# Performance work log

Hardware: AMD Instinct MI355X
Metric: run time of the kernel (lower is better)

## Reference

```python
import jax, jax.numpy as jnp
import numpy as np

F = 26            # number of categorical fields
V_FIELD = 8000    # vocab per field
V = F * V_FIELD   # 208000, size of every shared-index table
D_EMB = 16
DNN_IN = F * F * D_EMB  # 10816
H1, H2 = 256, 128
BS = 4096
NUM_DENSE = 13
EPS = 1e-5


def setup_inputs() -> dict:
    key = jax.random.key(0)
    ks = jax.random.split(key, 16)
    def n(k, shape, s=0.05):
        return jax.random.normal(k, shape, dtype=jnp.float32) * s
    return {
        "X_sparse": jax.random.randint(ks[0], (BS, F), 0, V_FIELD, dtype=jnp.int32),
        "X_dense": jax.random.normal(ks[1], (BS, NUM_DENSE), dtype=jnp.float32),
        "fm1_emb": n(ks[2], (V, 1)),
        "bias": jnp.zeros((1,), jnp.float32),
        "fm1_dense_W": n(ks[3], (1, NUM_DENSE)),
        "fm1_dense_b": jnp.zeros((1,), jnp.float32),
        "emb_tables": n(ks[4], (F, V, D_EMB)),  # one table per field (FFM)
        "dense_W": n(ks[5], (DNN_IN, NUM_DENSE)),
        "dense_b": jnp.zeros((DNN_IN,), jnp.float32),
        "W1": n(ks[6], (H1, DNN_IN)),
        "b1": jnp.zeros((H1,), jnp.float32),
        "g1": jnp.ones((H1,), jnp.float32),
        "beta1": jnp.zeros((H1,), jnp.float32),
        "W2": n(ks[7], (H2, H1)),
        "b2": jnp.zeros((H2,), jnp.float32),
        "g2": jnp.ones((H2,), jnp.float32),
        "beta2": jnp.zeros((H2,), jnp.float32),
        "Wout": n(ks[8], (1, H2)),
        "bout": jnp.zeros((1,), jnp.float32),
    }


def _bn(x, g, b):
    # BatchNorm1d in training mode: biased batch statistics
    m = jnp.mean(x, axis=0)
    v = jnp.var(x, axis=0)
    return (x - m) * jax.lax.rsqrt(v + EPS) * g + b


def reference(X_sparse, X_dense, fm1_emb, bias, fm1_dense_W, fm1_dense_b,
              emb_tables, dense_W, dense_b,
              W1, b1, g1, beta1, W2, b2, g2, beta2, Wout, bout):
    offsets = (jnp.arange(F, dtype=X_sparse.dtype) * V_FIELD)[None, :]
    X = X_sparse + offsets                      # [bs, F] global indices

    # FM first order
    fm1 = jnp.sum(fm1_emb[X], axis=1) + bias    # [bs, 1]
    fm1 = fm1 + X_dense @ fm1_dense_W.T + fm1_dense_b

    # FFM second order: E[t, b, f, d] = table t looked up at field f's index
    E = emb_tables[:, X, :]                     # [F, bs, F, d]
    A = jnp.transpose(E, (1, 0, 2, 3))          # [bs, F_table, F_field, d]
    # pair (i<j): xs[j][:, i] * xs[i][:, j] = A[b, i, j] * A[b, j, i]
    P = A * jnp.swapaxes(A, 1, 2)               # [bs, F, F, d]
    mask = jnp.triu(jnp.ones((F, F), jnp.float32), 1)
    fm2 = jnp.einsum('bijd,ij->b', P, mask)[:, None]  # [bs, 1]

    # DNN: concat per-table lookups then flatten -> [bs, F*F*d]
    dnn = A.reshape(A.shape[0], DNN_IN)
    dnn = dnn + jax.nn.relu(X_dense @ dense_W.T + dense_b)
    h = jax.nn.relu(_bn(dnn @ W1.T + b1, g1, beta1))  # dropout is identity (eval)
    h = jax.nn.relu(_bn(h @ W2.T + b2, g2, beta2))
    out = h @ Wout.T + bout
    return jax.nn.sigmoid(fm1 + fm2 + out)
```

## Files before the change

### kernel.cpp

```cpp
#include <hip/hip_runtime.h>

typedef __bf16 bf16x8 __attribute__((ext_vector_type(8)));
typedef float f32x4 __attribute__((ext_vector_type(4)));

#define F_FIELDS 26
#define V_FIELD  8000
#define V_TOT    208000
#define D_EMBD   16
#define DNN_IN   10816
#define BS       4096
#define ND       13
#define H1_DIM   256
#define H2_DIM   128
#define NP1      8

__device__ __forceinline__ unsigned short f2bf(float f) {
  unsigned u = __float_as_uint(f);
  u += 0x7fffu + ((u >> 16) & 1u);
  return (unsigned short)(u >> 16);
}
__device__ __forceinline__ float bf2f(unsigned short h) {
  return __uint_as_float(((unsigned)h) << 16);
}
__device__ __forceinline__ float bflo(unsigned u) { return __uint_as_float(u << 16); }
__device__ __forceinline__ float bfhi(unsigned u) { return __uint_as_float(u & 0xffff0000u); }
__device__ __forceinline__ unsigned packbf(float a, float b) {
  return (unsigned)f2bf(a) | ((unsigned)f2bf(b) << 16);
}

__device__ __forceinline__ void gload16(const void* g, void* l) {
  __builtin_amdgcn_global_load_lds(
      (const __attribute__((address_space(1))) unsigned int*)g,
      (__attribute__((address_space(3))) unsigned int*)l, 16, 0, 0);
}

__device__ __forceinline__ float dot8bf(uint4 a, uint4 b) {
  const unsigned* pa = (const unsigned*)&a;
  const unsigned* pb = (const unsigned*)&b;
  float s = 0.f;
#pragma unroll
  for (int k = 0; k < 4; ++k)
    s += bflo(pa[k]) * bflo(pb[k]) + bfhi(pa[k]) * bfhi(pb[k]);
  return s;
}

__global__ __launch_bounds__(256) void k_gather(
    const int* __restrict__ Xs, const float* __restrict__ emb,
    const float* __restrict__ fm1_emb, const float* __restrict__ bias,
    const float* __restrict__ fm1dW, const float* __restrict__ fm1db,
    const float* __restrict__ Xd,
    const float* __restrict__ W1, const float* __restrict__ W2,
    const float* __restrict__ dW, const float* __restrict__ db_,
    unsigned short* __restrict__ W1b, unsigned short* __restrict__ W2b,
    unsigned short* __restrict__ dWb,
    unsigned short* __restrict__ Abf, float* __restrict__ fm12) {
  const int b = blockIdx.x;
  const int tid = threadIdx.x;
  const int lane = tid & 63, wave = tid >> 6;
  __shared__ int   sidx[F_FIELDS];
  __shared__ float sc1[F_FIELDS];
  __shared__ __align__(16) unsigned short As[676 * 16];
  __shared__ float wred[4];

  if (tid < F_FIELDS) {
    int v = Xs[b * F_FIELDS + tid] + tid * V_FIELD;
    sidx[tid] = v;
    sc1[tid] = fm1_emb[v];
  }
  __syncthreads();

  const int q = tid & 3, rbase = tid >> 2;
  float4 vv[11];
#pragma unroll
  for (int it = 0; it < 11; ++it) {
    int r = rbase + it * 64;
    if (r < 676) {
      int i = r / 26, j = r - i * 26;
      const float* src = emb + ((size_t)i * V_TOT + sidx[j]) * D_EMBD + q * 4;
      vv[it] = *(const float4*)src;
    }
  }
  const int n1 = H1_DIM * DNN_IN, n2 = H2_DIM * H1_DIM;
  for (int t = b * 256 + tid; t < n1 + n2; t += BS * 256) {
    if (t < n1) W1b[t] = f2bf(W1[t]);
    else        W2b[t - n1] = f2bf(W2[t - n1]);
  }
  for (int e = b * 256 + tid; e < DNN_IN; e += BS * 256) {
    unsigned short row[32];
#pragma unroll
    for (int k = 0; k < 13; ++k) row[k] = f2bf(dW[e * 13 + k]);
    row[13] = f2bf(db_[e]);
#pragma unroll
    for (int k = 14; k < 32; ++k) row[k] = 0;
#pragma unroll
    for (int k = 0; k < 32; ++k) dWb[e * 32 + k] = row[k];
  }
#pragma unroll
  for (int it = 0; it < 11; ++it) {
    int r = rbase + it * 64;
    if (r < 676) {
      unsigned lo = packbf(vv[it].x, vv[it].y);
      unsigned hi = packbf(vv[it].z, vv[it].w);
      unsigned long long pk = (unsigned long long)lo |
                              ((unsigned long long)hi << 32);
      *(unsigned long long*)&As[r * 16 + q * 4] = pk;
      *(unsigned long long*)&Abf[(size_t)b * DNN_IN + r * 16 + q * 4] = pk;
    }
  }
  __syncthreads();

  float acc2 = 0.f;
  for (int p = tid; p < 325; p += 256) {
    float disc = sqrtf((float)(2601 - 8 * p));
    int i = (int)((51.f - disc) * 0.5f);
    int cum = 25 * i - ((i * (i - 1)) >> 1);
    int j = i + 1 + (p - cum);
    const unsigned short* r1 = &As[(i * 26 + j) * 16];
    const unsigned short* r2 = &As[(j * 26 + i) * 16];
    acc2 += dot8bf(*(const uint4*)r1, *(const uint4*)r2);
    acc2 += dot8bf(*(const uint4*)(r1 + 8), *(const uint4*)(r2 + 8));
  }
#pragma unroll
  for (int off = 32; off; off >>= 1) acc2 += __shfl_down(acc2, off);
  if (lane == 0) wred[wave] = acc2;
  __syncthreads();
  if (tid == 0) {
    float fm2 = wred[0] + wred[1] + wred[2] + wred[3];
    float f1 = bias[0] + fm1db[0];
#pragma unroll
    for (int j = 0; j < F_FIELDS; ++j) f1 += sc1[j];
    for (int k = 0; k < ND; ++k) f1 += Xd[b * ND + k] * fm1dW[k];
    fm12[b] = f1 + fm2;
  }
}

__global__ __launch_bounds__(256) void k_gemm1(
    const unsigned short* __restrict__ A, const unsigned short* __restrict__ B,
    const unsigned short* __restrict__ dWb, const float* __restrict__ Xd,
    unsigned short* __restrict__ C) {
  __shared__ __align__(16) unsigned short sA[3][64 * 32];
  __shared__ __align__(16) unsigned short sB[3][256 * 32];
  __shared__ __align__(16) unsigned short sWd[3][1024];
  __shared__ __align__(16) unsigned short sD[64 * 32];
  __shared__ __align__(16) unsigned short sXd[64 * 32];
  const int tid = threadIdx.x;
  const int lane = tid & 63, w = tid >> 6;
  const int id = blockIdx.x;
  const int p = id & 7, mt = id >> 3;
  const int m0 = mt * 64;
  const int s0 = (338 * p) >> 3, s1 = (338 * (p + 1)) >> 3;
  C += (size_t)p * ((size_t)BS * H1_DIM);

  if (tid < 64) {
    const float* xr = Xd + (size_t)(m0 + tid) * ND;
    unsigned short row[32];
#pragma unroll
    for (int k = 0; k < 13; ++k) row[k] = f2bf(xr[k]);
    row[13] = 0x3F80;
#pragma unroll
    for (int k = 14; k < 32; ++k) row[k] = 0;
#pragma unroll
    for (int k = 0; k < 32; ++k) sXd[tid * 32 + k] = row[k];
  }
  __syncthreads();

  const int q = tid & 3, rr = tid >> 2;
  const unsigned short* gA  = A + (size_t)(m0 + rr) * DNN_IN + q * 8;
  const unsigned short* gB0 = B + (size_t)rr * DNN_IN + q * 8;
  const int fr = lane & 15, fk = lane >> 4;
  const int oA = fr * 32 + fk * 8;
  const int oB = (w * 64 + fr) * 32 + fk * 8;

  const bf16x8 bvd = *(const bf16x8*)&sXd[(w * 16 + fr) * 32 + fk * 8];
  const int erow = (w * 16 + fr) * 32;
  const int ecol = fk * 4;

  f32x4 acc[4][4] = {};
  const f32x4 zf = {0.f, 0.f, 0.f, 0.f};

#define STAGE1(ks, bi) do { const int ko_ = (ks) * 32;                      \
    gload16(gA + ko_, &sA[bi][tid * 8]);                                    \
    gload16(gB0 + ko_, &sB[bi][tid * 8]);                                   \
    gload16(gB0 + (size_t)64 * DNN_IN + ko_, &sB[bi][2048 + tid * 8]);      \
    gload16(gB0 + (size_t)128 * DNN_IN + ko_, &sB[bi][4096 + tid * 8]);     \
    gload16(gB0 + (size_t)192 * DNN_IN + ko_, &sB[bi][6144 + tid * 8]);     \
    gload16(dWb + (size_t)ko_ * 32 + (size_t)lane * 8, &sWd[bi][lane * 8]); \
    gload16(dWb + (size_t)ko_ * 32 + 512 + (size_t)lane * 8,                \
            &sWd[bi][512 + lane * 8]); } while (0)

  STAGE1(s0, 0);
  if (s0 + 1 < s1) STAGE1(s0 + 1, 1);
  if (s0 + 2 < s1) STAGE1(s0 + 2, 2);

  int bi = 0;
  for (int ks = s0; ks < s1; ++ks) {
    if (ks + 2 < s1)      asm volatile("s_waitcnt vmcnt(14)" ::: "memory");
    else if (ks + 1 < s1) asm volatile("s_waitcnt vmcnt(7)" ::: "memory");
    else                  asm volatile("s_waitcnt vmcnt(0)" ::: "memory");
    __builtin_amdgcn_sched_barrier(0);
    __builtin_amdgcn_s_barrier();
    bf16x8 aw0 = *(const bf16x8*)&sWd[bi][fr * 32 + fk * 8];
    bf16x8 aw1 = *(const bf16x8*)&sWd[bi][(16 + fr) * 32 + fk * 8];
    bf16x8 bv[4];
#pragma unroll
    for (int ni = 0; ni < 4; ++ni) bv[ni] = *(const bf16x8*)&sB[bi][oB + ni * 512];
    uint2 a0 = *(const uint2*)&sA[bi][erow + ecol];
    uint2 a1 = *(const uint2*)&sA[bi][erow + 16 + ecol];
    asm volatile("s_waitcnt lgkmcnt(0)" ::: "memory");
    __builtin_amdgcn_sched_barrier(0);
    f32x4 d0 = __builtin_amdgcn_mfma_f32_16x16x32_bf16(aw0, bvd, zf, 0, 0, 0);
    f32x4 d1 = __builtin_amdgcn_mfma_f32_16x16x32_bf16(aw1, bvd, zf, 0, 0, 0);
    uint2 e0, e1;
    e0.x = packbf(bflo(a0.x) + fmaxf(d0[0], 0.f), bfhi(a0.x) + fmaxf(d0[1], 0.f));
    e0.y = packbf(bflo(a0.y) + fmaxf(d0[2], 0.f), bfhi(a0.y) + fmaxf(d0[3], 0.f));
    e1.x = packbf(bflo(a1.x) + fmaxf(d1[0], 0.f), bfhi(a1.x) + fmaxf(d1[1], 0.f));
    e1.y = packbf(bflo(a1.y) + fmaxf(d1[2], 0.f), bfhi(a1.y) + fmaxf(d1[3], 0.f));
    *(uint2*)&sD[erow + ecol] = e0;
    *(uint2*)&sD[erow + 16 + ecol] = e1;
    asm volatile("s_waitcnt lgkmcnt(0)" ::: "memory");
    __builtin_amdgcn_sched_barrier(0);
    __builtin_amdgcn_s_barrier();
    if (ks + 3 < s1) STAGE1(ks + 3, bi);
    bf16x8 ev[4];
#pragma unroll
    for (int mi = 0; mi < 4; ++mi) ev[mi] = *(const bf16x8*)&sD[oA + mi * 512];
    asm volatile("s_waitcnt lgkmcnt(0)" ::: "memory");
    __builtin_amdgcn_sched_barrier(0);
#pragma unroll
    for (int mi = 0; mi < 4; ++mi)
#pragma unroll
      for (int ni = 0; ni < 4; ++ni)
        acc[mi][ni] = __builtin_amdgcn_mfma_f32_16x16x32_bf16(
            ev[mi], bv[ni], acc[mi][ni], 0, 0, 0);
    bi = bi + 1; if (bi == 3) bi = 0;
  }
#pragma unroll
  for (int mi = 0; mi < 4; ++mi)
#pragma unroll
    for (int ni = 0; ni < 4; ++ni)
#pragma unroll
      for (int r = 0; r < 4; ++r) {
        int row = m0 + mi * 16 + fk * 4 + r;
        int col = w * 64 + ni * 16 + fr;
        C[(size_t)row * H1_DIM + col] = f2bf(acc[mi][ni][r]);
      }
#undef STAGE1
}

__global__ __launch_bounds__(256) void k_stat1(
    const unsigned short* __restrict__ Yp, const float* __restrict__ b1,
    float* __restrict__ ps, float* __restrict__ pq) {
  const int g = blockIdx.x, n = threadIdx.x;
  const size_t plane = (size_t)BS * H1_DIM;
  float s = 0.f, s2 = 0.f;
  float bn = b1[n];
  for (int bb = 0; bb < 16; ++bb) {
    size_t o = (size_t)(g * 16 + bb) * H1_DIM + n;
    float y = bn;
#pragma unroll
    for (int pp = 0; pp < NP1; ++pp) y += bf2f(Yp[o + pp * plane]);
    s += y; s2 += y * y;
  }
  ps[g * H1_DIM + n] = s;
  pq[g * H1_DIM + n] = s2;
}

__global__ __launch_bounds__(256) void k_apply1(
    const unsigned short* __restrict__ Yp, const float* __restrict__ b1,
    const float* __restrict__ ps, const float* __restrict__ pq,
    const float* __restrict__ g1, const float* __restrict__ be1,
    unsigned short* __restrict__ H1b) {
  const int g = blockIdx.x, n = threadIdx.x;
  const size_t plane = (size_t)BS * H1_DIM;
  float s = 0.f, s2 = 0.f;
  for (int gg = 0; gg < 256; ++gg) {
    s += ps[gg * H1_DIM + n];
    s2 += pq[gg * H1_DIM + n];
  }
  float m = s * (1.f / BS);
  float v = s2 * (1.f / BS) - m * m;
  float r = rsqrtf(v + 1e-5f);
  float ga = g1[n], bb_ = be1[n];
  float bn = b1[n];
  for (int bb = 0; bb < 16; ++bb) {
    size_t o = (size_t)(g * 16 + bb) * H1_DIM + n;
    float y = bn;
#pragma unroll
    for (int pp = 0; pp < NP1; ++pp) y += bf2f(Yp[o + pp * plane]);
    float h = (y - m) * r * ga + bb_;
    H1b[o] = f2bf(fmaxf(h, 0.f));
  }
}

__global__ __launch_bounds__(256) void k_gemm2(
    const unsigned short* __restrict__ A, const unsigned short* __restrict__ B,
    const float* __restrict__ b2, float* __restrict__ Y2,
    float* __restrict__ ps, float* __restrict__ pq) {
  __shared__ __align__(16) unsigned short sA[2][128 * 32];
  __shared__ __align__(16) unsigned short sB[2][128 * 32];
  __shared__ float redS[8][H2_DIM];
  __shared__ float redQ[8][H2_DIM];
  const int tid = threadIdx.x;
  const int lane = tid & 63, wave = tid >> 6;
  const int m0 = blockIdx.x * 128;

  const int q = tid & 3, rr = tid >> 2;
  const unsigned short* gA0 = A + (size_t)(m0 + rr) * H1_DIM + q * 8;
  const unsigned short* gA1 = gA0 + (size_t)64 * H1_DIM;
  const unsigned short* gB0 = B + (size_t)rr * H1_DIM + q * 8;
  const unsigned short* gB1 = gB0 + (size_t)64 * H1_DIM;
  const int lo = wave * 512;

  const int wr = wave >> 1, wc = wave & 1;
  const int fr = lane & 15, fk = lane >> 4;
  const int oA = (wr * 64 + fr) * 32 + fk * 8;
  const int oB = (wc * 64 + fr) * 32 + fk * 8;

  f32x4 acc[4][4] = {};
  {
    gload16(gA0, &sA[0][lo]);
    gload16(gA1, &sA[0][2048 + lo]);
    gload16(gB0, &sB[0][lo]);
    gload16(gB1, &sB[0][2048 + lo]);
  }
  for (int ks = 0; ks < 8; ++ks) {
    const int cur = ks & 1;
    if (ks + 1 < 8) {
      const int ko = (ks + 1) * 32;
      gload16(gA0 + ko, &sA[cur ^ 1][lo]);
      gload16(gA1 + ko, &sA[cur ^ 1][2048 + lo]);
      gload16(gB0 + ko, &sB[cur ^ 1][lo]);
      gload16(gB1 + ko, &sB[cur ^ 1][2048 + lo]);
      asm volatile("s_waitcnt vmcnt(4)" ::: "memory");
    } else {
      asm volatile("s_waitcnt vmcnt(0)" ::: "memory");
    }
    __builtin_amdgcn_sched_barrier(0);
    __builtin_amdgcn_s_barrier();
    bf16x8 av[4], bv[4];
#pragma unroll
    for (int mi = 0; mi < 4; ++mi) av[mi] = *(const bf16x8*)&sA[cur][oA + mi * 512];
#pragma unroll
    for (int ni = 0; ni < 4; ++ni) bv[ni] = *(const bf16x8*)&sB[cur][oB + ni * 512];
    asm volatile("s_waitcnt lgkmcnt(0)" ::: "memory");
    __builtin_amdgcn_sched_barrier(0);
    __builtin_amdgcn_s_barrier();
#pragma unroll
    for (int mi = 0; mi < 4; ++mi)
#pragma unroll
      for (int ni = 0; ni < 4; ++ni)
        acc[mi][ni] = __builtin_amdgcn_mfma_f32_16x16x32_bf16(
            av[mi], bv[ni], acc[mi][ni], 0, 0, 0);
  }
  float sc[4] = {0.f, 0.f, 0.f, 0.f}, sq[4] = {0.f, 0.f, 0.f, 0.f};
#pragma unroll
  for (int ni = 0; ni < 4; ++ni) {
    int col = wc * 64 + ni * 16 + fr;
    float bcol = b2[col];
#pragma unroll
    for (int mi = 0; mi < 4; ++mi)
#pragma unroll
      for (int r = 0; r < 4; ++r) {
        int row = m0 + wr * 64 + mi * 16 + fk * 4 + r;
        float y = acc[mi][ni][r] + bcol;
        Y2[(size_t)row * H2_DIM + col] = y;
        sc[ni] += y; sq[ni] += y * y;
      }
  }
  const int slot = wr * 4 + fk;
#pragma unroll
  for (int ni = 0; ni < 4; ++ni) {
    int col = wc * 64 + ni * 16 + fr;
    redS[slot][col] = sc[ni];
    redQ[slot][col] = sq[ni];
  }
  __syncthreads();
  if (tid < H2_DIM) {
    float s = 0.f, s2 = 0.f;
#pragma unroll
    for (int sl = 0; sl < 8; ++sl) { s += redS[sl][tid]; s2 += redQ[sl][tid]; }
    ps[blockIdx.x * H2_DIM + tid] = s;
    pq[blockIdx.x * H2_DIM + tid] = s2;
  }
}

__global__ __launch_bounds__(256) void k_final(
    const float* __restrict__ Y2, const float* __restrict__ ps,
    const float* __restrict__ pq, const float* __restrict__ g2,
    const float* __restrict__ be2, const float* __restrict__ Wout,
    const float* __restrict__ bout, const float* __restrict__ fm12,
    float* __restrict__ out) {
  const int tid = threadIdx.x, wave = tid >> 6, lane = tid & 63;
  __shared__ float sm[H2_DIM], sr[H2_DIM], sg[H2_DIM], sbe[H2_DIM], sw[H2_DIM];
  if (tid < H2_DIM) {
    float s = 0.f, s2 = 0.f;
    for (int g = 0; g < 32; ++g) {
      s += ps[g * H2_DIM + tid];
      s2 += pq[g * H2_DIM + tid];
    }
    float m = s * (1.f / BS);
    float v = s2 * (1.f / BS) - m * m;
    sm[tid] = m; sr[tid] = rsqrtf(v + 1e-5f);
    sg[tid] = g2[tid]; sbe[tid] = be2[tid]; sw[tid] = Wout[tid];
  }
  __syncthreads();
  const float bo = bout[0];
  for (int ii = 0; ii < 16; ++ii) {
    int s = blockIdx.x * 64 + wave * 16 + ii;
    float acc = 0.f;
#pragma unroll
    for (int nn = 0; nn < 2; ++nn) {
      int n = lane + nn * 64;
      float y = Y2[(size_t)s * H2_DIM + n];
      float h = (y - sm[n]) * sr[n] * sg[n] + sbe[n];
      acc += fmaxf(h, 0.f) * sw[n];
    }
#pragma unroll
    for (int off = 32; off; off >>= 1) acc += __shfl_down(acc, off);
    if (lane == 0) {
      float logit = fm12[s] + acc + bo;
      out[s] = 1.f / (1.f + expf(-logit));
    }
  }
}

extern "C" void kernel_launch(void* const* d_in, const int* in_sizes, int n_in,
                              void* d_out, int out_size, void* d_ws, size_t ws_size,
                              hipStream_t stream) {
  const int*   Xs     = (const int*)d_in[0];
  const float* Xd     = (const float*)d_in[1];
  const float* fm1e   = (const float*)d_in[2];
  const float* bias   = (const float*)d_in[3];
  const float* fm1dW  = (const float*)d_in[4];
  const float* fm1db  = (const float*)d_in[5];
  const float* emb    = (const float*)d_in[6];
  const float* dW     = (const float*)d_in[7];
  const float* db_    = (const float*)d_in[8];
  const float* W1     = (const float*)d_in[9];
  const float* b1     = (const float*)d_in[10];
  const float* g1     = (const float*)d_in[11];
  const float* be1    = (const float*)d_in[12];
  const float* W2     = (const float*)d_in[13];
  const float* b2     = (const float*)d_in[14];
  const float* g2     = (const float*)d_in[15];
  const float* be2    = (const float*)d_in[16];
  const float* Wout   = (const float*)d_in[17];
  const float* bout   = (const float*)d_in[18];
  float* out = (float*)d_out;

  char* w = (char*)d_ws;
  unsigned short* Dnn = (unsigned short*)w; w += (size_t)BS * DNN_IN * 2;
  unsigned short* W1b = (unsigned short*)w; w += (size_t)H1_DIM * DNN_IN * 2;
  unsigned short* W2b = (unsigned short*)w; w += (size_t)H2_DIM * H1_DIM * 2;
  unsigned short* dWb = (unsigned short*)w; w += (size_t)DNN_IN * 32 * 2;
  float* fm12 = (float*)w;  w += (size_t)BS * 4;
  unsigned short* Ypart = (unsigned short*)w; w += (size_t)NP1 * BS * H1_DIM * 2;
  unsigned short* H1b = (unsigned short*)w; w += (size_t)BS * H1_DIM * 2;
  float* Y2 = (float*)w;    w += (size_t)BS * H2_DIM * 4;
  float* ps1 = (float*)w;   w += 256 * H1_DIM * 4;
  float* pq1 = (float*)w;   w += 256 * H1_DIM * 4;
  float* ps2 = (float*)w;   w += 32 * H2_DIM * 4;
  float* pq2 = (float*)w;   w += 32 * H2_DIM * 4;

  k_gather<<<BS, 256, 0, stream>>>(Xs, emb, fm1e, bias, fm1dW, fm1db, Xd,
                                   W1, W2, dW, db_, W1b, W2b, dWb, Dnn, fm12);
  k_gemm1<<<64 * NP1, 256, 0, stream>>>(Dnn, W1b, dWb, Xd, Ypart);
  k_stat1<<<256, 256, 0, stream>>>(Ypart, b1, ps1, pq1);
  k_apply1<<<256, 256, 0, stream>>>(Ypart, b1, ps1, pq1, g1, be1, H1b);
  k_gemm2<<<32, 256, 0, stream>>>(H1b, W2b, b2, Y2, ps2, pq2);
  k_final<<<BS / 64, 256, 0, stream>>>(Y2, ps2, pq2, g2, be2, Wout, bout, fm12, out);
}
```

Before: 180.4 us.

## Fuse embedding gather into GEMM1 A-tile staging, drop DNN activation buffer

The gather kernel no longer writes the 4096x10816 bf16 DNN activation matrix to global memory. GEMM1 instead loads sparse indices into shared memory and gathers fp32 embedding rows directly from the tables into registers for each K-step. It converts them to bf16 and stores them into the A tile. The 3-stage loop is unrolled by 3 so each stage keeps its own register pair. This removes a large write and re-read of the activation buffer. The cost is that each of the 8 K-partition blocks re-gathers scattered embedding rows, and the waitcnt accounting changes.

```diff
diff --git a/kernel.cpp b/kernel.cpp
--- a/kernel.cpp
+++ b/kernel.cpp
@@ -52,8 +52,7 @@
     const float* __restrict__ W1, const float* __restrict__ W2,
     const float* __restrict__ dW, const float* __restrict__ db_,
     unsigned short* __restrict__ W1b, unsigned short* __restrict__ W2b,
-    unsigned short* __restrict__ dWb,
-    unsigned short* __restrict__ Abf, float* __restrict__ fm12) {
+    unsigned short* __restrict__ dWb, float* __restrict__ fm12) {
   const int b = blockIdx.x;
   const int tid = threadIdx.x;
   const int lane = tid & 63, wave = tid >> 6;
@@ -104,7 +103,6 @@
       unsigned long long pk = (unsigned long long)lo |
                               ((unsigned long long)hi << 32);
       *(unsigned long long*)&As[r * 16 + q * 4] = pk;
-      *(unsigned long long*)&Abf[(size_t)b * DNN_IN + r * 16 + q * 4] = pk;
     }
   }
   __syncthreads();
@@ -135,7 +133,8 @@
 }
 
 __global__ __launch_bounds__(256) void k_gemm1(
-    const unsigned short* __restrict__ A, const unsigned short* __restrict__ B,
+    const float* __restrict__ emb, const int* __restrict__ Xs,
+    const unsigned short* __restrict__ B,
     const unsigned short* __restrict__ dWb, const float* __restrict__ Xd,
     unsigned short* __restrict__ C) {
   __shared__ __align__(16) unsigned short sA[3][64 * 32];
@@ -143,6 +142,7 @@
   __shared__ __align__(16) unsigned short sWd[3][1024];
   __shared__ __align__(16) unsigned short sD[64 * 32];
   __shared__ __align__(16) unsigned short sXd[64 * 32];
+  __shared__ unsigned short sidx2[64 * 26];
   const int tid = threadIdx.x;
   const int lane = tid & 63, w = tid >> 6;
   const int id = blockIdx.x;
@@ -162,14 +162,18 @@
 #pragma unroll
     for (int k = 0; k < 32; ++k) sXd[tid * 32 + k] = row[k];
   }
-  __syncthreads();
-
-  const int q = tid & 3, rr = tid >> 2;
-  const unsigned short* gA  = A + (size_t)(m0 + rr) * DNN_IN + q * 8;
-  const unsigned short* gB0 = B + (size_t)rr * DNN_IN + q * 8;
+  for (int t = tid; t < 64 * F_FIELDS; t += 256)
+    sidx2[t] = (unsigned short)Xs[(size_t)m0 * F_FIELDS + t];
+  __syncthreads();
+
   const int fr = lane & 15, fk = lane >> 4;
   const int oA = fr * 32 + fk * 8;
   const int oB = (w * 64 + fr) * 32 + fk * 8;
+  const int rr = tid >> 2, q = tid & 3;
+  const unsigned short* gB0 = B + (size_t)rr * DNN_IN + q * 8;
+
+  const int hQ = tid >> 7, prQ = (tid >> 6) & 1, sQ = tid & 63;
+  const int sAoff = sQ * 32 + prQ * 16 + hQ * 8;
 
   const bf16x8 bvd = *(const bf16x8*)&sXd[(w * 16 + fr) * 32 + fk * 8];
   const int erow = (w * 16 + fr) * 32;
@@ -177,62 +181,81 @@
 
   f32x4 acc[4][4] = {};
   const f32x4 zf = {0.f, 0.f, 0.f, 0.f};
-
-#define STAGE1(ks, bi) do { const int ko_ = (ks) * 32;                      \
-    gload16(gA + ko_, &sA[bi][tid * 8]);                                    \
-    gload16(gB0 + ko_, &sB[bi][tid * 8]);                                   \
-    gload16(gB0 + (size_t)64 * DNN_IN + ko_, &sB[bi][2048 + tid * 8]);      \
-    gload16(gB0 + (size_t)128 * DNN_IN + ko_, &sB[bi][4096 + tid * 8]);     \
-    gload16(gB0 + (size_t)192 * DNN_IN + ko_, &sB[bi][6144 + tid * 8]);     \
-    gload16(dWb + (size_t)ko_ * 32 + (size_t)lane * 8, &sWd[bi][lane * 8]); \
+  float4 A0a = {0,0,0,0}, A0b = {0,0,0,0};
+  float4 A1a = {0,0,0,0}, A1b = {0,0,0,0};
+  float4 A2a = {0,0,0,0}, A2b = {0,0,0,0};
+
+#define STAGE1(ks_, bi_, Ra, Rb) do { const int ko_ = (ks_) * 32;           \
+    const int r_ = 2 * (ks_) + prQ;                                         \
+    const int i_ = r_ / 26, j_ = r_ - i_ * 26;                              \
+    const int v_ = j_ * V_FIELD + (int)sidx2[sQ * 26 + j_];                 \
+    const float* ga_ = emb + ((size_t)i_ * V_TOT + v_) * D_EMBD + hQ * 8;   \
+    Ra = *(const float4*)ga_;                                               \
+    Rb = *(const float4*)(ga_ + 4);                                         \
+    gload16(gB0 + ko_, &sB[bi_][tid * 8]);                                  \
+    gload16(gB0 + (size_t)64 * DNN_IN + ko_, &sB[bi_][2048 + tid * 8]);     \
+    gload16(gB0 + (size_t)128 * DNN_IN + ko_, &sB[bi_][4096 + tid * 8]);    \
+    gload16(gB0 + (size_t)192 * DNN_IN + ko_, &sB[bi_][6144 + tid * 8]);    \
+    gload16(dWb + (size_t)ko_ * 32 + (size_t)lane * 8, &sWd[bi_][lane * 8]);\
     gload16(dWb + (size_t)ko_ * 32 + 512 + (size_t)lane * 8,                \
-            &sWd[bi][512 + lane * 8]); } while (0)
-
-  STAGE1(s0, 0);
-  if (s0 + 1 < s1) STAGE1(s0 + 1, 1);
-  if (s0 + 2 < s1) STAGE1(s0 + 2, 2);
-
-  int bi = 0;
-  for (int ks = s0; ks < s1; ++ks) {
-    if (ks + 2 < s1)      asm volatile("s_waitcnt vmcnt(14)" ::: "memory");
-    else if (ks + 1 < s1) asm volatile("s_waitcnt vmcnt(7)" ::: "memory");
-    else                  asm volatile("s_waitcnt vmcnt(0)" ::: "memory");
-    __builtin_amdgcn_sched_barrier(0);
-    __builtin_amdgcn_s_barrier();
-    bf16x8 aw0 = *(const bf16x8*)&sWd[bi][fr * 32 + fk * 8];
-    bf16x8 aw1 = *(const bf16x8*)&sWd[bi][(16 + fr) * 32 + fk * 8];
-    bf16x8 bv[4];
-#pragma unroll
-    for (int ni = 0; ni < 4; ++ni) bv[ni] = *(const bf16x8*)&sB[bi][oB + ni * 512];
-    uint2 a0 = *(const uint2*)&sA[bi][erow + ecol];
-    uint2 a1 = *(const uint2*)&sA[bi][erow + 16 + ecol];
-    asm volatile("s_waitcnt lgkmcnt(0)" ::: "memory");
-    __builtin_amdgcn_sched_barrier(0);
-    f32x4 d0 = __builtin_amdgcn_mfma_f32_16x16x32_bf16(aw0, bvd, zf, 0, 0, 0);
-    f32x4 d1 = __builtin_amdgcn_mfma_f32_16x16x32_bf16(aw1, bvd, zf, 0, 0, 0);
-    uint2 e0, e1;
-    e0.x = packbf(bflo(a0.x) + fmaxf(d0[0], 0.f), bfhi(a0.x) + fmaxf(d0[1], 0.f));
-    e0.y = packbf(bflo(a0.y) + fmaxf(d0[2], 0.f), bfhi(a0.y) + fmaxf(d0[3], 0.f));
-    e1.x = packbf(bflo(a1.x) + fmaxf(d1[0], 0.f), bfhi(a1.x) + fmaxf(d1[1], 0.f));
-    e1.y = packbf(bflo(a1.y) + fmaxf(d1[2], 0.f), bfhi(a1.y) + fmaxf(d1[3], 0.f));
-    *(uint2*)&sD[erow + ecol] = e0;
-    *(uint2*)&sD[erow + 16 + ecol] = e1;
-    asm volatile("s_waitcnt lgkmcnt(0)" ::: "memory");
-    __builtin_amdgcn_sched_barrier(0);
-    __builtin_amdgcn_s_barrier();
-    if (ks + 3 < s1) STAGE1(ks + 3, bi);
-    bf16x8 ev[4];
-#pragma unroll
-    for (int mi = 0; mi < 4; ++mi) ev[mi] = *(const bf16x8*)&sD[oA + mi * 512];
-    asm volatile("s_waitcnt lgkmcnt(0)" ::: "memory");
-    __builtin_amdgcn_sched_barrier(0);
-#pragma unroll
-    for (int mi = 0; mi < 4; ++mi)
-#pragma unroll
-      for (int ni = 0; ni < 4; ++ni)
-        acc[mi][ni] = __builtin_amdgcn_mfma_f32_16x16x32_bf16(
-            ev[mi], bv[ni], acc[mi][ni], 0, 0, 0);
-    bi = bi + 1; if (bi == 3) bi = 0;
+            &sWd[bi_][512 + lane * 8]); } while (0)
+
+#define BODY(ks_, bi_, Ra, Rb) do {                                         \
+    if ((ks_) + 2 < s1)      asm volatile("s_waitcnt vmcnt(16)" ::: "memory"); \
+    else if ((ks_) + 1 < s1) asm volatile("s_waitcnt vmcnt(8)" ::: "memory");  \
+    else                     asm volatile("s_waitcnt vmcnt(0)" ::: "memory");  \
+    __builtin_amdgcn_sched_barrier(0);                                      \
+    { uint4 pk_; pk_.x = packbf(Ra.x, Ra.y); pk_.y = packbf(Ra.z, Ra.w);    \
+      pk_.z = packbf(Rb.x, Rb.y); pk_.w = packbf(Rb.z, Rb.w);               \
+      *(uint4*)&sA[bi_][sAoff] = pk_; }                                     \
+    asm volatile("s_waitcnt lgkmcnt(0)" ::: "memory");                      \
+    __builtin_amdgcn_sched_barrier(0);                                      \
+    __builtin_amdgcn_s_barrier();                \
+    bf16x8 aw0 = *(const bf16x8*)&sWd[bi_][fr * 32 + fk * 8];               \
+    bf16x8 aw1 = *(const bf16x8*)&sWd[bi_][(16 + fr) * 32 + fk * 8];        \
+    bf16x8 bv[4];                                                           \
+    _Pragma("unroll")                                                       \
+    for (int ni = 0; ni < 4; ++ni)                                          \
+      bv[ni] = *(const bf16x8*)&sB[bi_][oB + ni * 512];                     \
+    uint2 a0 = *(const uint2*)&sA[bi_][erow + ecol];                        \
+    uint2 a1 = *(const uint2*)&sA[bi_][erow + 16 + ecol];                   \
+    asm volatile("s_waitcnt lgkmcnt(0)" ::: "memory");                      \
+    __builtin_amdgcn_sched_barrier(0);                                      \
+    f32x4 d0 = __builtin_amdgcn_mfma_f32_16x16x32_bf16(aw0, bvd, zf, 0, 0, 0); \
+    f32x4 d1 = __builtin_amdgcn_mfma_f32_16x16x32_bf16(aw1, bvd, zf, 0, 0, 0); \
+    uint2 e0, e1;                                                           \
+    e0.x = packbf(bflo(a0.x) + fmaxf(d0[0], 0.f), bfhi(a0.x) + fmaxf(d0[1], 0.f)); \
+    e0.y = packbf(bflo(a0.y) + fmaxf(d0[2], 0.f), bfhi(a0.y) + fmaxf(d0[3], 0.f)); \
+    e1.x = packbf(bflo(a1.x) + fmaxf(d1[0], 0.f), bfhi(a1.x) + fmaxf(d1[1], 0.f)); \
+    e1.y = packbf(bflo(a1.y) + fmaxf(d1[2], 0.f), bfhi(a1.y) + fmaxf(d1[3], 0.f)); \
+    *(uint2*)&sD[erow + ecol] = e0;                                         \
+    *(uint2*)&sD[erow + 16 + ecol] = e1;                                    \
+    asm volatile("s_waitcnt lgkmcnt(0)" ::: "memory");                      \
+    __builtin_amdgcn_sched_barrier(0);                                      \
+    __builtin_amdgcn_s_barrier();                 \
+    if ((ks_) + 3 < s1) STAGE1((ks_) + 3, bi_, Ra, Rb);                     \
+    bf16x8 ev[4];                                                           \
+    _Pragma("unroll")                                                       \
+    for (int mi = 0; mi < 4; ++mi)                                          \
+      ev[mi] = *(const bf16x8*)&sD[oA + mi * 512];                          \
+    asm volatile("s_waitcnt lgkmcnt(0)" ::: "memory");                      \
+    __builtin_amdgcn_sched_barrier(0);                                      \
+    _Pragma("unroll")                                                       \
+    for (int mi = 0; mi < 4; ++mi)                                          \
+      _Pragma("unroll")                                                     \
+      for (int ni = 0; ni < 4; ++ni)                                        \
+        acc[mi][ni] = __builtin_amdgcn_mfma_f32_16x16x32_bf16(              \
+            ev[mi], bv[ni], acc[mi][ni], 0, 0, 0);                          \
+  } while (0)
+
+  STAGE1(s0, 0, A0a, A0b);
+  STAGE1(s0 + 1, 1, A1a, A1b);
+  STAGE1(s0 + 2, 2, A2a, A2b);
+
+  for (int base = s0; base < s1; base += 3) {
+    BODY(base, 0, A0a, A0b);
+    if (base + 1 < s1) BODY(base + 1, 1, A1a, A1b);
+    if (base + 2 < s1) BODY(base + 2, 2, A2a, A2b);
   }
 #pragma unroll
   for (int mi = 0; mi < 4; ++mi)
@@ -245,6 +268,7 @@
         C[(size_t)row * H1_DIM + col] = f2bf(acc[mi][ni][r]);
       }
 #undef STAGE1
+#undef BODY
 }
 
 __global__ __launch_bounds__(256) void k_stat1(
@@ -449,7 +473,6 @@
   float* out = (float*)d_out;
 
   char* w = (char*)d_ws;
-  unsigned short* Dnn = (unsigned short*)w; w += (size_t)BS * DNN_IN * 2;
   unsigned short* W1b = (unsigned short*)w; w += (size_t)H1_DIM * DNN_IN * 2;
   unsigned short* W2b = (unsigned short*)w; w += (size_t)H2_DIM * H1_DIM * 2;
   unsigned short* dWb = (unsigned short*)w; w += (size_t)DNN_IN * 32 * 2;
@@ -463,8 +486,8 @@
   float* pq2 = (float*)w;   w += 32 * H2_DIM * 4;
 
   k_gather<<<BS, 256, 0, stream>>>(Xs, emb, fm1e, bias, fm1dW, fm1db, Xd,
-                                   W1, W2, dW, db_, W1b, W2b, dWb, Dnn, fm12);
-  k_gemm1<<<64 * NP1, 256, 0, stream>>>(Dnn, W1b, dWb, Xd, Ypart);
+                                   W1, W2, dW, db_, W1b, W2b, dWb, fm12);
+  k_gemm1<<<64 * NP1, 256, 0, stream>>>(emb, Xs, W1b, dWb, Xd, Ypart);
   k_stat1<<<256, 256, 0, stream>>>(Ypart, b1, ps1, pq1);
   k_apply1<<<256, 256, 0, stream>>>(Ypart, b1, ps1, pq1, g1, be1, H1b);
   k_gemm2<<<32, 256, 0, stream>>>(H1b, W2b, b2, Y2, ps2, pq2);
```

Result: slower. 192.5 us (+6.7%).
